# Kernel tuning notes

Measured on AMD Instinct MI355X. Metric: run time of the kernel, lower is better.

Reference implementation:

```python
import jax, jax.numpy as jnp
import numpy as np

N = 512

def setup_inputs() -> dict:
    key = jax.random.key(0)
    ks = jax.random.split(key, 7)
    def rn(k, shape, fan_in):
        # kaiming-ish scale so activations stay sane
        return jax.random.normal(k, shape, dtype=jnp.float32) / np.sqrt(max(fan_in, 1))
    return {
        "x": jax.random.normal(ks[0], (N,), dtype=jnp.float32),
        "W1": rn(ks[1], (2, 1024), 2),
        "b1": rn(ks[2], (1024,), 1024),
        "W2": rn(ks[3], (1024, 128), 1024),
        "b2": rn(ks[4], (128,), 128),
        "W3": rn(ks[5], (128, 1), 128),
        "b3": rn(ks[6], (1,), 1),
    }


def reference(x, W1, b1, W2, b2, W3, b3):
    n = x.shape[0]
    # all (t_i, t_j) pairs: [N, N, 2]
    pairs = jnp.stack(
        [jnp.broadcast_to(x[:, None], (n, n)),
         jnp.broadcast_to(x[None, :], (n, n))], axis=-1)
    # batched 3-layer MLP over all pairs
    h = jax.nn.relu(jnp.einsum("ijc,ch->ijh", pairs, W1) + b1)   # [N,N,1024]
    h = jax.nn.relu(jnp.einsum("ijh,hk->ijk", h, W2) + b2)       # [N,N,128]
    out = (jnp.einsum("ijk,ko->ijo", h, W3) + b3)[..., 0]        # [N,N]
    # original fills only j >= i (diagonal overwritten from eye); lower stays 0
    K = jnp.triu(out)
    return K.T @ K
```

## Files before the change

kernel.cpp:

```cpp
#include <hip/hip_runtime.h>
#include <hip/hip_fp16.h>

typedef _Float16 f16;
typedef _Float16 f16x8 __attribute__((ext_vector_type(8)));
typedef float f32x4 __attribute__((ext_vector_type(4)));

__device__ __forceinline__ f16x8 relu8(f16x8 a) {
#if __has_builtin(__builtin_elementwise_max)
  return __builtin_elementwise_max(a, (f16x8)(f16)0);
#else
  f16x8 r;
#pragma unroll
  for (int i = 0; i < 8; i++) r[i] = a[i] > (f16)0 ? a[i] : (f16)0;
  return r;
#endif
}

__device__ __forceinline__ f16x8 bcast8(f16 s) {
  return (f16x8){s, s, s, s, s, s, s, s};
}

__device__ __forceinline__ void atomAddF(float* p, float v) {
#if defined(__AMDGCN__)
  unsafeAtomicAdd(p, v);
#else
  atomicAdd(p, v);
#endif
}

__global__ __launch_bounds__(512, 2) void k_fused(
    const float* __restrict__ x, const float* __restrict__ W1,
    const float* __restrict__ b1, const float* __restrict__ b2,
    const float* __restrict__ W3, const float* __restrict__ b3,
    const float* __restrict__ W2,
    float* __restrict__ Kp0, float* __restrict__ Kp1,
    float* __restrict__ C) {
  __shared__ f16 w2f[65536];
  __shared__ f16 w1af[1024], b1f[1024], w1bf[1024];
  __shared__ f16 hat[8192];
  __shared__ f16 xs[512];

  const int tid = threadIdx.x;
  const int lane = tid & 63, wv = tid >> 6;
  const int cL = lane & 15, q = lane >> 4;

  {
    float2 z = {0.f, 0.f};
    ((float2*)C)[blockIdx.x * 512 + tid] = z;
  }

  if (tid < 128) {
    const int c8 = tid << 3;
    const float4 a0 = *(const float4*)(W1 + c8);
    const float4 a1 = *(const float4*)(W1 + c8 + 4);
    const float4 g0 = *(const float4*)(b1 + c8);
    const float4 g1 = *(const float4*)(b1 + c8 + 4);
    f16x8 oa, og;
    oa[0] = (f16)a0.x; oa[1] = (f16)a0.y; oa[2] = (f16)a0.z; oa[3] = (f16)a0.w;
    oa[4] = (f16)a1.x; oa[5] = (f16)a1.y; oa[6] = (f16)a1.z; oa[7] = (f16)a1.w;
    og[0] = (f16)g0.x; og[1] = (f16)g0.y; og[2] = (f16)g0.z; og[3] = (f16)g0.w;
    og[4] = (f16)g1.x; og[5] = (f16)g1.y; og[6] = (f16)g1.z; og[7] = (f16)g1.w;
    *(f16x8*)(&w1af[c8]) = oa;
    *(f16x8*)(&b1f[c8]) = og;
  } else if (tid < 256) {
    const int c8 = (tid - 128) << 3;
    const float4 a0 = *(const float4*)(W1 + 1024 + c8);
    const float4 a1 = *(const float4*)(W1 + 1024 + c8 + 4);
    f16x8 ob;
    ob[0] = (f16)a0.x; ob[1] = (f16)a0.y; ob[2] = (f16)a0.z; ob[3] = (f16)a0.w;
    ob[4] = (f16)a1.x; ob[5] = (f16)a1.y; ob[6] = (f16)a1.z; ob[7] = (f16)a1.w;
    *(f16x8*)(&w1bf[c8]) = ob;
  } else if (tid < 320) {
    const int c8 = (tid - 256) << 3;
    const float4 x0 = *(const float4*)(x + c8);
    const float4 x1 = *(const float4*)(x + c8 + 4);
    f16x8 ox;
    ox[0] = (f16)x0.x; ox[1] = (f16)x0.y; ox[2] = (f16)x0.z; ox[3] = (f16)x0.w;
    ox[4] = (f16)x1.x; ox[5] = (f16)x1.y; ox[6] = (f16)x1.z; ox[7] = (f16)x1.w;
    *(f16x8*)(&xs[c8]) = ox;
  }

  int cur_nh = -1;

  for (int t = (int)blockIdx.x; t < 320; t += 256) {
    int nh, jt, s;
    if (t < 64 || t >= 256) {
      const int b = (t < 64) ? t : (t - 256);
      nh = b & 1;
      const int jd = b >> 1;
      const int jt1 = jd >> 4, l = jd & 15;
      if (t < 64) { jt = jt1;            s = jt * 16 + l; }
      else        { jt = (jt1 + 2) & 3;  s = jt * 16 + (15 - l); }
    } else {
      const int f = t - 64;
      nh = f & 1;
      const int jf = f >> 1;
      if (jf < 16)      { jt = 1; s = jf; }
      else if (jf < 48) { jt = 2; s = jf - 16; }
      else              { jt = 3; s = jf - 48; }
    }
    const int i0 = s << 3, j0 = jt << 7;
    float* __restrict__ Kp = nh ? Kp1 : Kp0;

    __syncthreads();
    if (nh != cur_nh) {
      #pragma unroll
      for (int p = 0; p < 16; p++) {
        const int sl = p * 512 + tid;
        const int frag = sl >> 6, l = sl & 63;
        const int cgL = frag >> 5, kb2 = frag & 31;
        const int q2 = l >> 4, cL2 = l & 15;
        const int n = nh * 64 + cgL * 16 + cL2;
        const float* src = W2 + (kb2 * 32 + q2 * 8) * 128 + n;
        f16x8 o;
        #pragma unroll
        for (int e = 0; e < 8; e++) o[e] = (f16)src[e * 128];
        *(f16x8*)(&w2f[frag * 512 + l * 8]) = o;
      }
      cur_nh = nh;
    }
    {
      const int il_s = tid >> 6, kb = (tid & 63) << 4;
      const f16x8 xv = bcast8(xs[i0 + il_s]);
      const f16x8 wa0 = *(const f16x8*)(&w1af[kb]);
      const f16x8 wa1 = *(const f16x8*)(&w1af[kb + 8]);
      const f16x8 bb0 = *(const f16x8*)(&b1f[kb]);
      const f16x8 bb1 = *(const f16x8*)(&b1f[kb + 8]);
      *(f16x8*)(&hat[il_s * 1024 + kb])     = xv * wa0 + bb0;
      *(f16x8*)(&hat[il_s * 1024 + kb + 8]) = xv * wa1 + bb1;
    }
    __syncthreads();

    const int i = i0 + wv;
    const int dij = i - j0;
    const int rgmin = (dij > 0) ? (dij >> 4) : 0;

    f16 xjs[8];
    #pragma unroll
    for (int rg = 0; rg < 8; rg++) xjs[rg] = xs[j0 + rg * 16 + cL];

    f32x4 acc[8][4];
    #pragma unroll
    for (int rg = 0; rg < 8; rg++)
      #pragma unroll
      for (int cg = 0; cg < 4; cg++) acc[rg][cg] = (f32x4){0.f, 0.f, 0.f, 0.f};

    const f16* hrow  = hat + wv * 1024 + q * 8;
    const f16* wrow  = w1bf + q * 8;
    const f16* bbase = w2f + lane * 8;

    for (int kk = 0; kk < 32; ++kk) {
      const f16x8 hv = *(const f16x8*)(hrow + kk * 32);
      const f16x8 wb = *(const f16x8*)(wrow + kk * 32);
      f16x8 bf[4];
      #pragma unroll
      for (int cg = 0; cg < 4; cg++)
        bf[cg] = *(const f16x8*)(bbase + (cg * 32 + kk) * 512);
      #pragma unroll
      for (int rg = 0; rg < 8; rg++) {
        if (rg >= rgmin) {
          const f16x8 af = relu8(bcast8(xjs[rg]) * wb + hv);
          #pragma unroll
          for (int cg = 0; cg < 4; cg++)
            acc[rg][cg] = __builtin_amdgcn_mfma_f32_16x16x32_f16(af, bf[cg], acc[rg][cg], 0, 0, 0);
        }
      }
    }

    float b2v[4], w3v[4];
    #pragma unroll
    for (int cg = 0; cg < 4; cg++) {
      b2v[cg] = b2[nh * 64 + cg * 16 + cL];
      w3v[cg] = W3[nh * 64 + cg * 16 + cL];
    }
    const float badd = (nh == 0) ? b3[0] : 0.f;
    #pragma unroll
    for (int rg = 0; rg < 8; rg++) {
      if (rg >= rgmin) {
        #pragma unroll
        for (int r = 0; r < 4; r++) {
          float ssum = 0.f;
          #pragma unroll
          for (int cg = 0; cg < 4; cg++)
            ssum = fmaf(fmaxf(acc[rg][cg][r] + b2v[cg], 0.f), w3v[cg], ssum);
          ssum += __shfl_xor(ssum, 1, 64);
          ssum += __shfl_xor(ssum, 2, 64);
          ssum += __shfl_xor(ssum, 4, 64);
          ssum += __shfl_xor(ssum, 8, 64);
          if (cL == 0) {
            const int j = j0 + rg * 16 + q * 4 + r;
            if (j >= i) Kp[i * 512 + j] = ssum + badd;
          }
        }
      }
    }
  }
}

__global__ __launch_bounds__(256) void k_atta2(const float* __restrict__ K0,
                                               const float* __restrict__ K1,
                                               float* __restrict__ C) {
  __shared__ float sp[32 * 36], sq[32 * 36];
  int a = 0, rem = (int)blockIdx.x;
  #pragma unroll
  for (int aa = 0; aa < 16; aa++) {
    const int c = (16 - aa) * (aa + 1);
    if (rem < c) { a = aa; break; }
    rem -= c;
  }
  const int b = a + rem / (a + 1);
  const int ic = rem % (a + 1);
  const int pb = a * 32, qb = b * 32, i0 = ic * 32;

  const int tid = threadIdx.x;
  const int ii = tid >> 3, p4 = (tid & 7) << 2;
  const int irow = i0 + ii;
  {
    const int gp = irow * 512 + pb + p4, gq = irow * 512 + qb + p4;
    const float4 a0 = *(const float4*)(K0 + gp);
    const float4 a1 = *(const float4*)(K1 + gp);
    const float4 b0 = *(const float4*)(K0 + gq);
    const float4 b1 = *(const float4*)(K1 + gq);
    float vp[4] = {a0.x + a1.x, a0.y + a1.y, a0.z + a1.z, a0.w + a1.w};
    float vq[4] = {b0.x + b1.x, b0.y + b1.y, b0.z + b1.z, b0.w + b1.w};
    #pragma unroll
    for (int e = 0; e < 4; e++) {
      sp[ii * 36 + p4 + e] = (irow <= pb + p4 + e) ? vp[e] : 0.f;
      sq[ii * 36 + p4 + e] = (irow <= qb + p4 + e) ? vq[e] : 0.f;
    }
  }
  __syncthreads();

  const int tx = tid & 15, ty = tid >> 4;
  float c00 = 0.f, c01 = 0.f, c10 = 0.f, c11 = 0.f;
  #pragma unroll 8
  for (int k = 0; k < 32; k++) {
    const float a0 = sp[k * 36 + ty * 2], a1 = sp[k * 36 + ty * 2 + 1];
    const float b0 = sq[k * 36 + tx * 2], b1 = sq[k * 36 + tx * 2 + 1];
    c00 = fmaf(a0, b0, c00); c01 = fmaf(a0, b1, c01);
    c10 = fmaf(a1, b0, c10); c11 = fmaf(a1, b1, c11);
  }
  const int p0 = pb + ty * 2, q0 = qb + tx * 2;
  atomAddF(&C[p0 * 512 + q0], c00);       atomAddF(&C[p0 * 512 + q0 + 1], c01);
  atomAddF(&C[(p0 + 1) * 512 + q0], c10); atomAddF(&C[(p0 + 1) * 512 + q0 + 1], c11);
  if (pb != qb) {
    atomAddF(&C[q0 * 512 + p0], c00);       atomAddF(&C[(q0 + 1) * 512 + p0], c01);
    atomAddF(&C[q0 * 512 + p0 + 1], c10);   atomAddF(&C[(q0 + 1) * 512 + p0 + 1], c11);
  }
}

extern "C" void kernel_launch(void* const* d_in, const int* in_sizes, int n_in,
                              void* d_out, int out_size, void* d_ws, size_t ws_size,
                              hipStream_t stream) {
  const float* x  = (const float*)d_in[0];
  const float* W1 = (const float*)d_in[1];
  const float* b1 = (const float*)d_in[2];
  const float* W2 = (const float*)d_in[3];
  const float* b2 = (const float*)d_in[4];
  const float* W3 = (const float*)d_in[5];
  const float* b3 = (const float*)d_in[6];
  float* out = (float*)d_out;
  char* ws = (char*)d_ws;

  float* Kp0 = (float*)ws;
  float* Kp1 = (float*)(ws + (1 << 20));

  k_fused<<<256, 512, 0, stream>>>(x, W1, b1, b2, W3, b3, W2, Kp0, Kp1, out);
  k_atta2<<<816, 256, 0, stream>>>(Kp0, Kp1, out);
}
```

Before: 120.6 us.

## Replace split-K atomic Gram accumulation with per-tile K loop and direct stores

The K^T K stage no longer splits the reduction dimension across blocks with float atomics. Each of the 136 upper-triangle tiles now loops over its chunks with double-buffered shared memory and prefetches the next chunk while computing. It then writes its result (and the mirrored tile) with plain stores, so the output no longer has to be zeroed inside the MLP kernel. This removes atomic traffic and the zeroing writes, but leaves fewer, unevenly loaded blocks: the last tile row loops 16 chunks while the first does one.

```diff
diff --git a/kernel.cpp b/kernel.cpp
--- a/kernel.cpp
+++ b/kernel.cpp
@@ -20,21 +20,12 @@
   return (f16x8){s, s, s, s, s, s, s, s};
 }
 
-__device__ __forceinline__ void atomAddF(float* p, float v) {
-#if defined(__AMDGCN__)
-  unsafeAtomicAdd(p, v);
-#else
-  atomicAdd(p, v);
-#endif
-}
-
 __global__ __launch_bounds__(512, 2) void k_fused(
     const float* __restrict__ x, const float* __restrict__ W1,
     const float* __restrict__ b1, const float* __restrict__ b2,
     const float* __restrict__ W3, const float* __restrict__ b3,
     const float* __restrict__ W2,
-    float* __restrict__ Kp0, float* __restrict__ Kp1,
-    float* __restrict__ C) {
+    float* __restrict__ Kp0, float* __restrict__ Kp1) {
   __shared__ f16 w2f[65536];
   __shared__ f16 w1af[1024], b1f[1024], w1bf[1024];
   __shared__ f16 hat[8192];
@@ -43,11 +34,6 @@
   const int tid = threadIdx.x;
   const int lane = tid & 63, wv = tid >> 6;
   const int cL = lane & 15, q = lane >> 4;
-
-  {
-    float2 z = {0.f, 0.f};
-    ((float2*)C)[blockIdx.x * 512 + tid] = z;
-  }
 
   if (tid < 128) {
     const int c8 = tid << 3;
@@ -200,52 +186,76 @@
 __global__ __launch_bounds__(256) void k_atta2(const float* __restrict__ K0,
                                                const float* __restrict__ K1,
                                                float* __restrict__ C) {
-  __shared__ float sp[32 * 36], sq[32 * 36];
+  __shared__ __align__(16) float sp[2][32 * 36];
+  __shared__ __align__(16) float sq[2][32 * 36];
+
   int a = 0, rem = (int)blockIdx.x;
   #pragma unroll
   for (int aa = 0; aa < 16; aa++) {
-    const int c = (16 - aa) * (aa + 1);
+    const int c = 16 - aa;
     if (rem < c) { a = aa; break; }
     rem -= c;
   }
-  const int b = a + rem / (a + 1);
-  const int ic = rem % (a + 1);
-  const int pb = a * 32, qb = b * 32, i0 = ic * 32;
+  const int b = a + rem;
+  const int pb = a * 32, qb = b * 32;
+  const int nchunk = a + 1;
 
   const int tid = threadIdx.x;
   const int ii = tid >> 3, p4 = (tid & 7) << 2;
-  const int irow = i0 + ii;
+  const int tx = tid & 15, ty = tid >> 4;
+
+  float4 x0, x1, y0, y1;
   {
-    const int gp = irow * 512 + pb + p4, gq = irow * 512 + qb + p4;
-    const float4 a0 = *(const float4*)(K0 + gp);
-    const float4 a1 = *(const float4*)(K1 + gp);
-    const float4 b0 = *(const float4*)(K0 + gq);
-    const float4 b1 = *(const float4*)(K1 + gq);
-    float vp[4] = {a0.x + a1.x, a0.y + a1.y, a0.z + a1.z, a0.w + a1.w};
-    float vq[4] = {b0.x + b1.x, b0.y + b1.y, b0.z + b1.z, b0.w + b1.w};
-    #pragma unroll
-    for (int e = 0; e < 4; e++) {
-      sp[ii * 36 + p4 + e] = (irow <= pb + p4 + e) ? vp[e] : 0.f;
-      sq[ii * 36 + p4 + e] = (irow <= qb + p4 + e) ? vq[e] : 0.f;
-    }
-  }
-  __syncthreads();
-
-  const int tx = tid & 15, ty = tid >> 4;
+    const int gp = ii * 512 + pb + p4, gq = ii * 512 + qb + p4;
+    x0 = *(const float4*)(K0 + gp);
+    x1 = *(const float4*)(K1 + gp);
+    y0 = *(const float4*)(K0 + gq);
+    y1 = *(const float4*)(K1 + gq);
+  }
+
   float c00 = 0.f, c01 = 0.f, c10 = 0.f, c11 = 0.f;
-  #pragma unroll 8
-  for (int k = 0; k < 32; k++) {
-    const float a0 = sp[k * 36 + ty * 2], a1 = sp[k * 36 + ty * 2 + 1];
-    const float b0 = sq[k * 36 + tx * 2], b1 = sq[k * 36 + tx * 2 + 1];
-    c00 = fmaf(a0, b0, c00); c01 = fmaf(a0, b1, c01);
-    c10 = fmaf(a1, b0, c10); c11 = fmaf(a1, b1, c11);
-  }
+
+  for (int ic = 0; ic < nchunk; ic++) {
+    float* __restrict__ spb = sp[ic & 1];
+    float* __restrict__ sqb = sq[ic & 1];
+    const int r = ic * 32 + ii;
+    float4 vp, vq;
+    vp.x = (r <= pb + p4 + 0) ? x0.x + x1.x : 0.f;
+    vp.y = (r <= pb + p4 + 1) ? x0.y + x1.y : 0.f;
+    vp.z = (r <= pb + p4 + 2) ? x0.z + x1.z : 0.f;
+    vp.w = (r <= pb + p4 + 3) ? x0.w + x1.w : 0.f;
+    vq.x = (r <= qb + p4 + 0) ? y0.x + y1.x : 0.f;
+    vq.y = (r <= qb + p4 + 1) ? y0.y + y1.y : 0.f;
+    vq.z = (r <= qb + p4 + 2) ? y0.z + y1.z : 0.f;
+    vq.w = (r <= qb + p4 + 3) ? y0.w + y1.w : 0.f;
+    *(float4*)&spb[ii * 36 + p4] = vp;
+    *(float4*)&sqb[ii * 36 + p4] = vq;
+    __syncthreads();
+
+    if (ic + 1 < nchunk) {
+      const int r2 = (ic + 1) * 32 + ii;
+      const int gp = r2 * 512 + pb + p4, gq = r2 * 512 + qb + p4;
+      x0 = *(const float4*)(K0 + gp);
+      x1 = *(const float4*)(K1 + gp);
+      y0 = *(const float4*)(K0 + gq);
+      y1 = *(const float4*)(K1 + gq);
+    }
+
+    #pragma unroll 8
+    for (int k = 0; k < 32; k++) {
+      const float2 av = *(const float2*)&spb[k * 36 + ty * 2];
+      const float2 bv = *(const float2*)&sqb[k * 36 + tx * 2];
+      c00 = fmaf(av.x, bv.x, c00); c01 = fmaf(av.x, bv.y, c01);
+      c10 = fmaf(av.y, bv.x, c10); c11 = fmaf(av.y, bv.y, c11);
+    }
+  }
+
   const int p0 = pb + ty * 2, q0 = qb + tx * 2;
-  atomAddF(&C[p0 * 512 + q0], c00);       atomAddF(&C[p0 * 512 + q0 + 1], c01);
-  atomAddF(&C[(p0 + 1) * 512 + q0], c10); atomAddF(&C[(p0 + 1) * 512 + q0 + 1], c11);
+  *(float2*)&C[p0 * 512 + q0]       = make_float2(c00, c01);
+  *(float2*)&C[(p0 + 1) * 512 + q0] = make_float2(c10, c11);
   if (pb != qb) {
-    atomAddF(&C[q0 * 512 + p0], c00);       atomAddF(&C[(q0 + 1) * 512 + p0], c01);
-    atomAddF(&C[q0 * 512 + p0 + 1], c10);   atomAddF(&C[(q0 + 1) * 512 + p0 + 1], c11);
+    *(float2*)&C[q0 * 512 + p0]       = make_float2(c00, c10);
+    *(float2*)&C[(q0 + 1) * 512 + p0] = make_float2(c01, c11);
   }
 }
 
@@ -265,6 +275,6 @@
   float* Kp0 = (float*)ws;
   float* Kp1 = (float*)(ws + (1 << 20));
 
-  k_fused<<<256, 512, 0, stream>>>(x, W1, b1, b2, W3, b3, W2, Kp0, Kp1, out);
-  k_atta2<<<816, 256, 0, stream>>>(Kp0, Kp1, out);
-}
+  k_fused<<<256, 512, 0, stream>>>(x, W1, b1, b2, W3, b3, W2, Kp0, Kp1);
+  k_atta2<<<136, 256, 0, stream>>>(Kp0, Kp1, out);
+}
```

After: 119.2 us. Within noise of the previous version (-1.1%).
